# Performance work log

Measured on AMD Instinct MI355X. Metric: run time of the kernel, lower is better.

Reference implementation:

```python
import jax, jax.numpy as jnp
import numpy as np

N = 50000          # number of nodes / output rows (len(degs))
IN_C, OUT_C = 16, 16
EDGE_F = 13        # edge feature dim fed to filter net
HID = 32           # filter-net hidden width
E_NOMINAL = 800000 # target number of edges (sum of degs)


def setup_inputs() -> dict:
    rng = np.random.default_rng(0)
    # variable per-node degrees in [0, 32], adjusted so they sum exactly to E_NOMINAL
    degs = rng.integers(0, 33, size=N).astype(np.int64)
    degs[0] = max(0, degs[0] + (E_NOMINAL - int(degs.sum())))
    E = int(degs.sum())
    # segment id of each edge = destination node (equivalent to the degs-driven loop)
    idxd = np.repeat(np.arange(N, dtype=np.int32), degs)
    idxn = rng.integers(0, N, size=E).astype(np.int32)  # source node gather index

    key = jax.random.key(0)
    k1, k2, k3, k4 = jax.random.split(key, 4)
    x = jax.random.normal(k1, (N, IN_C), jnp.float32)
    edgefeats = jax.random.normal(k2, (E, EDGE_F), jnp.float32)
    # filter net: Linear(EDGE_F->HID) -> ReLU -> Linear(HID->IN_C*OUT_C)
    W1 = jax.random.normal(k3, (EDGE_F, HID), jnp.float32) / np.float32(np.sqrt(EDGE_F))
    b1 = jnp.zeros((HID,), jnp.float32)
    W2 = jax.random.normal(k4, (HID, IN_C * OUT_C), jnp.float32) / np.float32(np.sqrt(HID))
    b2 = jnp.zeros((IN_C * OUT_C,), jnp.float32)
    return {
        "x": x, "edgefeats": edgefeats,
        "W1": W1, "b1": b1, "W2": W2, "b2": b2,
        "idxn": jnp.asarray(idxn), "idxd": jnp.asarray(idxd),
        "degs": jnp.asarray(degs.astype(np.float32)),
    }


def reference(x, edgefeats, W1, b1, W2, b2, idxn, idxd, degs):
    # filter net generates a per-edge [IN_C, OUT_C] weight matrix
    h = jax.nn.relu(edgefeats @ W1 + b1)                 # [E, HID]
    w = (h @ W2 + b2).reshape(-1, IN_C, OUT_C)           # [E, IN_C, OUT_C]
    # gather source-node features and apply per-edge matvec (bmm with [E,1,IN_C])
    sel = x[idxn]                                        # [E, IN_C]
    prod = jnp.einsum('ei,eio->eo', sel, w)              # [E, OUT_C]
    # segment-mean over each node's incoming edges; degree-0 nodes -> 0
    s = jax.ops.segment_sum(prod, idxd, num_segments=N)  # [N, OUT_C]
    d = degs[:, None]
    return jnp.where(d > 0, s / jnp.maximum(d, 1.0), jnp.float32(0.0))
```

## Files before the change

kernel.cpp:

```cpp
#include <hip/hip_runtime.h>

typedef _Float16 half2v __attribute__((ext_vector_type(2)));
typedef _Float16 half4v __attribute__((ext_vector_type(4)));
typedef _Float16 half8v __attribute__((ext_vector_type(8)));
typedef float   float4v __attribute__((ext_vector_type(4)));

#define INC     16
#define OUTC    16
#define EFN     13
#define HIDC    32
#define EPW     128
#define WPB     4
#define MAXSPAN 40

#define GLOBAL_AS __attribute__((address_space(1)))
#define LDS_AS    __attribute__((address_space(3)))

union H8 { half8v v; half2v h2[4]; };

__global__ __launch_bounds__(256) void prep(
    const float* __restrict__ W2,
    const float* __restrict__ x,
    _Float16*    __restrict__ wsB,
    _Float16*    __restrict__ wsXh,
    float*       __restrict__ out,
    int nh)
{
    const int b = blockIdx.x;
    if (b < 32) {
        const int i = b * 256 + threadIdx.x;
        const int j = i & 7;
        const int l = (i >> 3) & 63;
        const int t = i >> 9;
        const int q = l >> 4, n = l & 15;
        const int kk = (j < 4) ? (q * 4 + j) : (16 + q * 4 + (j & 3));
        wsB[i] = (_Float16)W2[kk * 256 + t * 16 + n];
    } else {
        const int i = (b - 32) * 256 + threadIdx.x;
        if (i * 4 < nh)
            ((float4*)out)[i] = make_float4(0, 0, 0, 0);
        if (i * 8 < nh) {
            const float4 v0 = ((const float4*)x)[i * 2];
            const float4 v1 = ((const float4*)x)[i * 2 + 1];
            half8v h;
            h[0] = (_Float16)v0.x; h[1] = (_Float16)v0.y;
            h[2] = (_Float16)v0.z; h[3] = (_Float16)v0.w;
            h[4] = (_Float16)v1.x; h[5] = (_Float16)v1.y;
            h[6] = (_Float16)v1.z; h[7] = (_Float16)v1.w;
            *(half8v*)(wsXh + (size_t)i * 8) = h;
        }
    }
}

__global__ __launch_bounds__(256, 3) void edge_kernel(
    const _Float16* __restrict__ xh,
    const float* __restrict__ edgefeats,
    const float* __restrict__ W1,
    const float* __restrict__ b1,
    const float* __restrict__ b2,
    const int*   __restrict__ idxn,
    const int*   __restrict__ idxd,
    const float* __restrict__ degs,
    const _Float16* __restrict__ wsB,
    float*       __restrict__ out,
    int E)
{
    __shared__ __align__(16) float sEF[WPB][EPW * EFN];
    __shared__ __align__(16) int   sidxn[WPB][EPW];
    __shared__ float lacc[WPB][MAXSPAN * OUTC];

    const int tid  = threadIdx.x;
    const int lane = tid & 63;
    const int wid  = tid >> 6;
    const int n    = lane & 15;
    const int q    = lane >> 4;

    const long vw = (long)blockIdx.x * WPB + wid;
    const long b0 = vw * EPW;
    if (b0 >= (long)E) return;
    const long bEnd = (b0 + EPW < (long)E) ? (b0 + EPW) : (long)E;
    const bool full = (b0 + EPW <= (long)E);
    const long Em1  = (long)E - 1;

    float* sEF_w   = sEF[wid];
    int*   sidxn_w = sidxn[wid];
    float* lacc_w  = lacc[wid];

    const long ea = b0 + n, eb = b0 + 16 + n;
    const int nd0 = idxn[(ea <= Em1) ? ea : Em1];
    const int nd1 = idxn[(eb <= Em1) ? eb : Em1];
    __builtin_amdgcn_sched_barrier(0);

    if (full) {
        const char* efsrc = (const char*)edgefeats + (size_t)b0 * (EFN * 4);
        #pragma unroll
        for (int c = 0; c < 6; ++c)
            __builtin_amdgcn_global_load_lds(
                (const GLOBAL_AS unsigned int*)(efsrc + c * 1024 + lane * 16),
                (LDS_AS unsigned int*)((char*)sEF_w + c * 1024), 16, 0, 0);
        if (lane < 32) {
            __builtin_amdgcn_global_load_lds(
                (const GLOBAL_AS unsigned int*)(efsrc + 6144 + lane * 16),
                (LDS_AS unsigned int*)((char*)sEF_w + 6144), 16, 0, 0);
            __builtin_amdgcn_global_load_lds(
                (const GLOBAL_AS unsigned int*)((const char*)(idxn + b0) + lane * 16),
                (LDS_AS unsigned int*)sidxn_w, 16, 0, 0);
        }
    } else {
        const long mx = (long)E * EFN - 1;
        for (int i = lane; i < EPW * EFN; i += 64) {
            long gi = b0 * EFN + i;
            if (gi > mx) gi = mx;
            sEF_w[i] = edgefeats[gi];
        }
        for (int i = lane; i < EPW; i += 64) {
            long e = b0 + i;
            if (e > Em1) e = Em1;
            sidxn_w[i] = idxn[e];
        }
    }
    __builtin_amdgcn_sched_barrier(0);

    const int d_lo = idxd[b0];
    const int d_hi = idxd[bEnd - 1];
    const int span = d_hi - d_lo;

    H8 bfr[16];
    #pragma unroll
    for (int t = 0; t < 16; ++t)
        bfr[t].v = *(const half8v*)(wsB + ((size_t)(t * 64 + lane) * 8));

    #pragma unroll
    for (int it = 0; it < MAXSPAN * OUTC / 64; ++it) lacc_w[lane + it * 64] = 0.0f;

    half4v a1, a2;
    float4v c1, c2;
    #pragma unroll
    for (int jj = 0; jj < 4; ++jj) {
        const int f = q * 4 + jj;
        const bool ok = (f < EFN);
        a1[jj] = ok ? (_Float16)W1[f * HIDC + n]      : (_Float16)0.f;
        a2[jj] = ok ? (_Float16)W1[f * HIDC + 16 + n] : (_Float16)0.f;
        c1[jj] = b1[q * 4 + jj];
        c2[jj] = b1[16 + q * 4 + jj];
    }
    half8v bfragB2;
    #pragma unroll
    for (int j = 0; j < 8; ++j) {
        _Float16 val = (_Float16)0.f;
        if (q < 2) val = (_Float16)b2[(q * 8 + j) * 16 + n];
        bfragB2[j] = val;
    }

    const int f0i = (q < 3) ? (q * 4) : 9;

    half8v pxa0 = *(const half8v*)(xh + (size_t)nd0 * INC);
    half8v pxb0 = *(const half8v*)(xh + (size_t)nd0 * INC + 8);
    half8v pxa1 = *(const half8v*)(xh + (size_t)nd1 * INC);
    half8v pxb1 = *(const half8v*)(xh + (size_t)nd1 * INC + 8);
    __builtin_amdgcn_sched_barrier(0);

    asm volatile("s_waitcnt vmcnt(0) lgkmcnt(0)" ::: "memory");
    __builtin_amdgcn_sched_barrier(0);

    #pragma unroll
    for (int t16 = 0; t16 < 8; ++t16) {
        const long base = b0 + (long)t16 * 16;
        const bool vM   = (base + n < (long)E);

        const half8v xA = (t16 & 1) ? pxa1 : pxa0;
        const half8v xB = (t16 & 1) ? pxb1 : pxb0;
        if (t16 < 6) {
            const int ndn = sidxn_w[(t16 + 2) * 16 + n];
            if (t16 & 1) {
                pxa1 = *(const half8v*)(xh + (size_t)ndn * INC);
                pxb1 = *(const half8v*)(xh + (size_t)ndn * INC + 8);
            } else {
                pxa0 = *(const half8v*)(xh + (size_t)ndn * INC);
                pxb0 = *(const half8v*)(xh + (size_t)ndn * INC + 8);
            }
        }
        long de = base + q * 4;
        if (de > (long)E - 4) de = (long)E - 4;
        const int4 dd = *(const int4*)(idxd + de);
        __builtin_amdgcn_sched_barrier(0);

        const float* efp = sEF_w + (size_t)(t16 * 16 + n) * EFN + f0i;
        const float e0 = efp[0], e1 = efp[1], e2 = efp[2], e3 = efp[3];

        H8 sa, sb_;
        sa.v = xA; sb_.v = xB;
        const half2v zz = {(_Float16)0.f, (_Float16)0.f};
        half2v selh[8];
        #pragma unroll
        for (int i = 0; i < 4; ++i) {
            selh[i]     = vM ? sa.h2[i]  : zz;
            selh[4 + i] = vM ? sb_.h2[i] : zz;
        }

        half4v efB;
        if (q < 3) {
            efB[0] = (_Float16)e0; efB[1] = (_Float16)e1;
            efB[2] = (_Float16)e2; efB[3] = (_Float16)e3;
        } else {
            efB[0] = (_Float16)e3; efB[1] = (_Float16)0.f;
            efB[2] = (_Float16)0.f; efB[3] = (_Float16)0.f;
        }

        const float4v hf1 = __builtin_amdgcn_mfma_f32_16x16x16f16(a1, efB, c1, 0, 0, 0);
        const float4v hf2 = __builtin_amdgcn_mfma_f32_16x16x16f16(a2, efB, c2, 0, 0, 0);

        H8 hu;
        #pragma unroll
        for (int r = 0; r < 2; ++r) {
            half2v t1 = {(_Float16)fmaxf(hf1[2*r], 0.f), (_Float16)fmaxf(hf1[2*r+1], 0.f)};
            half2v t2 = {(_Float16)fmaxf(hf2[2*r], 0.f), (_Float16)fmaxf(hf2[2*r+1], 0.f)};
            hu.h2[r]     = t1;
            hu.h2[2 + r] = t2;
        }

        float4v acc = {0.f, 0.f, 0.f, 0.f};
        #pragma unroll
        for (int t = 0; t < 16; ++t) {
            _Float16 sv = (t & 1) ? selh[t >> 1][1] : selh[t >> 1][0];
            half2v sb = {sv, sv};
            H8 a;
            a.h2[0] = sb * hu.h2[0];
            a.h2[1] = sb * hu.h2[1];
            a.h2[2] = sb * hu.h2[2];
            a.h2[3] = sb * hu.h2[3];
            acc = __builtin_amdgcn_mfma_f32_16x16x32_f16(a.v, bfr[t].v, acc, 0, 0, 0);
        }
        {
            H8 a;
            #pragma unroll
            for (int j2 = 0; j2 < 4; ++j2) {
                a.h2[j2] = (q < 2) ? selh[q * 4 + j2] : zz;
            }
            acc = __builtin_amdgcn_mfma_f32_16x16x32_f16(a.v, bfragB2, acc, 0, 0, 0);
        }

        const int r0 = ((dd.x < d_hi) ? dd.x : d_hi) - d_lo;
        const int r1 = ((dd.y < d_hi) ? dd.y : d_hi) - d_lo;
        const int r2 = ((dd.z < d_hi) ? dd.z : d_hi) - d_lo;
        const int r3 = ((dd.w < d_hi) ? dd.w : d_hi) - d_lo;
        if (r0 == r3) {
            atomicAdd(&lacc_w[r0 * OUTC + n], acc[0] + acc[1] + acc[2] + acc[3]);
        } else {
            atomicAdd(&lacc_w[r0 * OUTC + n], acc[0]);
            atomicAdd(&lacc_w[r1 * OUTC + n], acc[1]);
            atomicAdd(&lacc_w[r2 * OUTC + n], acc[2]);
            atomicAdd(&lacc_w[r3 * OUTC + n], acc[3]);
        }
    }

    asm volatile("s_waitcnt lgkmcnt(0)" ::: "memory");

    const bool first_starts = (b0 == 0)        || (idxd[b0 - 1] != d_lo);
    const bool last_ends    = (bEnd == (long)E) || (idxd[bEnd]   != d_hi);

    for (int i = lane; i < (span + 1) * OUTC; i += 64) {
        const int u = i >> 4;
        const int o = i & 15;
        const int v = d_lo + u;
        const float bin = lacc_w[u * OUTC + o];
        const bool starts = (u > 0)    || first_starts;
        const bool ends   = (u < span) || last_ends;
        const float dg = degs[v];
        const float val = (dg > 0.0f) ? bin / dg : 0.0f;
        if (starts && ends) {
            out[(size_t)v * OUTC + o] = val;
        } else {
            atomicAdd(&out[(size_t)v * OUTC + o], val);
        }
    }
}

extern "C" void kernel_launch(void* const* d_in, const int* in_sizes, int n_in,
                              void* d_out, int out_size, void* d_ws, size_t ws_size,
                              hipStream_t stream)
{
    const float* x         = (const float*)d_in[0];
    const float* edgefeats = (const float*)d_in[1];
    const float* W1        = (const float*)d_in[2];
    const float* b1        = (const float*)d_in[3];
    const float* W2        = (const float*)d_in[4];
    const float* b2        = (const float*)d_in[5];
    const int*   idxn      = (const int*)d_in[6];
    const int*   idxd      = (const int*)d_in[7];
    const float* degs      = (const float*)d_in[8];

    const int E = in_sizes[6];
    const int N = in_sizes[8];
    const int nvw   = (E + EPW - 1) / EPW;
    const int gridw = (nvw + WPB - 1) / WPB;
    const int nh = N * INC;

    _Float16* wsB  = (_Float16*)d_ws;
    _Float16* wsXh = (_Float16*)((char*)d_ws + 16384);

    const int zblocks = (nh / 4 + 255) / 256;
    prep<<<32 + zblocks, 256, 0, stream>>>(W2, x, wsB, wsXh, (float*)d_out, nh);

    edge_kernel<<<gridw, 256, 0, stream>>>(wsXh, edgefeats, W1, b1, b2,
                                           idxn, idxd, degs, wsB,
                                           (float*)d_out, E);
}
```

Measured before the change: 158.1 us.

## Double edges per wave to 256 and loop tiles with paired prefetch macro

Each wave now processes 256 edges instead of 128 (16 tiles of 16). The edge-feature async copy grows to 13 full chunks, and the per-tile body becomes a macro invoked in a non-unrolled loop over tile pairs with double-buffered x prefetch. Launch bounds drop from 3 to 2 blocks per CU to fit the larger LDS footprint, and MAXSPAN rises to 48. The aim is to amortize per-wave setup (W1/W2 fragment loads, flush of local bins) over more edges, at the cost of occupancy and a higher risk of a wave's segment span overflowing the LDS bins.

Result: slower. 170.1 us (+7.6%).

```diff
diff --git a/kernel.cpp b/kernel.cpp
--- a/kernel.cpp
+++ b/kernel.cpp
@@ -9,9 +9,10 @@
 #define OUTC    16
 #define EFN     13
 #define HIDC    32
-#define EPW     128
+#define EPW     256
+#define NT      (EPW / 16)
 #define WPB     4
-#define MAXSPAN 40
+#define MAXSPAN 48
 
 #define GLOBAL_AS __attribute__((address_space(1)))
 #define LDS_AS    __attribute__((address_space(3)))
@@ -52,7 +53,86 @@
     }
 }
 
-__global__ __launch_bounds__(256, 3) void edge_kernel(
+#define DO_TILE(T16, PXA, PXB)                                               \
+  {                                                                          \
+    const long base = b0 + (long)(T16) * 16;                                 \
+    const bool vM   = (base + n < (long)E);                                  \
+    const half8v xA = PXA;                                                   \
+    const half8v xB = PXB;                                                   \
+    const int pft = (T16) + 2;                                               \
+    if (pft < NT) {                                                          \
+        const int ndn = sidxn_w[pft * 16 + n];                               \
+        PXA = *(const half8v*)(xh + (size_t)ndn * INC);                      \
+        PXB = *(const half8v*)(xh + (size_t)ndn * INC + 8);                  \
+    }                                                                        \
+    long de = base + q * 4;                                                  \
+    if (de > (long)E - 4) de = (long)E - 4;                                  \
+    const int4 dd = *(const int4*)(idxd + de);                               \
+    __builtin_amdgcn_sched_barrier(0);                                       \
+    const float* efp = sEF_w + (size_t)((T16) * 16 + n) * EFN + f0i;         \
+    const float e0 = efp[0], e1 = efp[1], e2 = efp[2], e3 = efp[3];          \
+    H8 sa, sb_;                                                              \
+    sa.v = xA; sb_.v = xB;                                                   \
+    const half2v zz = {(_Float16)0.f, (_Float16)0.f};                        \
+    half2v selh[8];                                                          \
+    _Pragma("unroll")                                                        \
+    for (int i = 0; i < 4; ++i) {                                            \
+        selh[i]     = vM ? sa.h2[i]  : zz;                                   \
+        selh[4 + i] = vM ? sb_.h2[i] : zz;                                   \
+    }                                                                        \
+    half4v efB;                                                              \
+    if (q < 3) {                                                             \
+        efB[0] = (_Float16)e0; efB[1] = (_Float16)e1;                        \
+        efB[2] = (_Float16)e2; efB[3] = (_Float16)e3;                        \
+    } else {                                                                 \
+        efB[0] = (_Float16)e3; efB[1] = (_Float16)0.f;                       \
+        efB[2] = (_Float16)0.f; efB[3] = (_Float16)0.f;                      \
+    }                                                                        \
+    const float4v hf1 = __builtin_amdgcn_mfma_f32_16x16x16f16(a1, efB, c1, 0, 0, 0); \
+    const float4v hf2 = __builtin_amdgcn_mfma_f32_16x16x16f16(a2, efB, c2, 0, 0, 0); \
+    H8 hu;                                                                   \
+    _Pragma("unroll")                                                        \
+    for (int r = 0; r < 2; ++r) {                                            \
+        half2v t1 = {(_Float16)fmaxf(hf1[2*r], 0.f), (_Float16)fmaxf(hf1[2*r+1], 0.f)}; \
+        half2v t2 = {(_Float16)fmaxf(hf2[2*r], 0.f), (_Float16)fmaxf(hf2[2*r+1], 0.f)}; \
+        hu.h2[r]     = t1;                                                   \
+        hu.h2[2 + r] = t2;                                                   \
+    }                                                                        \
+    float4v acc = {0.f, 0.f, 0.f, 0.f};                                      \
+    _Pragma("unroll")                                                        \
+    for (int t = 0; t < 16; ++t) {                                           \
+        _Float16 sv = (t & 1) ? selh[t >> 1][1] : selh[t >> 1][0];           \
+        half2v sb = {sv, sv};                                                \
+        H8 a;                                                                \
+        a.h2[0] = sb * hu.h2[0];                                             \
+        a.h2[1] = sb * hu.h2[1];                                             \
+        a.h2[2] = sb * hu.h2[2];                                             \
+        a.h2[3] = sb * hu.h2[3];                                             \
+        acc = __builtin_amdgcn_mfma_f32_16x16x32_f16(a.v, bfr[t].v, acc, 0, 0, 0); \
+    }                                                                        \
+    {                                                                        \
+        H8 a;                                                                \
+        _Pragma("unroll")                                                    \
+        for (int j2 = 0; j2 < 4; ++j2) {                                     \
+            a.h2[j2] = (q < 2) ? selh[q * 4 + j2] : zz;                      \
+        }                                                                    \
+        acc = __builtin_amdgcn_mfma_f32_16x16x32_f16(a.v, bfragB2, acc, 0, 0, 0); \
+    }                                                                        \
+    const int r0 = ((dd.x < d_hi) ? dd.x : d_hi) - d_lo;                     \
+    const int r1 = ((dd.y < d_hi) ? dd.y : d_hi) - d_lo;                     \
+    const int r2 = ((dd.z < d_hi) ? dd.z : d_hi) - d_lo;                     \
+    const int r3 = ((dd.w < d_hi) ? dd.w : d_hi) - d_lo;                     \
+    if (r0 == r3) {                                                          \
+        atomicAdd(&lacc_w[r0 * OUTC + n], acc[0] + acc[1] + acc[2] + acc[3]);\
+    } else {                                                                 \
+        atomicAdd(&lacc_w[r0 * OUTC + n], acc[0]);                           \
+        atomicAdd(&lacc_w[r1 * OUTC + n], acc[1]);                           \
+        atomicAdd(&lacc_w[r2 * OUTC + n], acc[2]);                           \
+        atomicAdd(&lacc_w[r3 * OUTC + n], acc[3]);                           \
+    }                                                                        \
+  }
+
+__global__ __launch_bounds__(256, 2) void edge_kernel(
     const _Float16* __restrict__ xh,
     const float* __restrict__ edgefeats,
     const float* __restrict__ W1,
@@ -94,18 +174,13 @@
     if (full) {
         const char* efsrc = (const char*)edgefeats + (size_t)b0 * (EFN * 4);
         #pragma unroll
-        for (int c = 0; c < 6; ++c)
+        for (int c = 0; c < 13; ++c)
             __builtin_amdgcn_global_load_lds(
                 (const GLOBAL_AS unsigned int*)(efsrc + c * 1024 + lane * 16),
                 (LDS_AS unsigned int*)((char*)sEF_w + c * 1024), 16, 0, 0);
-        if (lane < 32) {
-            __builtin_amdgcn_global_load_lds(
-                (const GLOBAL_AS unsigned int*)(efsrc + 6144 + lane * 16),
-                (LDS_AS unsigned int*)((char*)sEF_w + 6144), 16, 0, 0);
-            __builtin_amdgcn_global_load_lds(
-                (const GLOBAL_AS unsigned int*)((const char*)(idxn + b0) + lane * 16),
-                (LDS_AS unsigned int*)sidxn_w, 16, 0, 0);
-        }
+        __builtin_amdgcn_global_load_lds(
+            (const GLOBAL_AS unsigned int*)((const char*)(idxn + b0) + lane * 16),
+            (LDS_AS unsigned int*)sidxn_w, 16, 0, 0);
     } else {
         const long mx = (long)E * EFN - 1;
         for (int i = lane; i < EPW * EFN; i += 64) {
@@ -163,95 +238,9 @@
     asm volatile("s_waitcnt vmcnt(0) lgkmcnt(0)" ::: "memory");
     __builtin_amdgcn_sched_barrier(0);
 
-    #pragma unroll
-    for (int t16 = 0; t16 < 8; ++t16) {
-        const long base = b0 + (long)t16 * 16;
-        const bool vM   = (base + n < (long)E);
-
-        const half8v xA = (t16 & 1) ? pxa1 : pxa0;
-        const half8v xB = (t16 & 1) ? pxb1 : pxb0;
-        if (t16 < 6) {
-            const int ndn = sidxn_w[(t16 + 2) * 16 + n];
-            if (t16 & 1) {
-                pxa1 = *(const half8v*)(xh + (size_t)ndn * INC);
-                pxb1 = *(const half8v*)(xh + (size_t)ndn * INC + 8);
-            } else {
-                pxa0 = *(const half8v*)(xh + (size_t)ndn * INC);
-                pxb0 = *(const half8v*)(xh + (size_t)ndn * INC + 8);
-            }
-        }
-        long de = base + q * 4;
-        if (de > (long)E - 4) de = (long)E - 4;
-        const int4 dd = *(const int4*)(idxd + de);
-        __builtin_amdgcn_sched_barrier(0);
-
-        const float* efp = sEF_w + (size_t)(t16 * 16 + n) * EFN + f0i;
-        const float e0 = efp[0], e1 = efp[1], e2 = efp[2], e3 = efp[3];
-
-        H8 sa, sb_;
-        sa.v = xA; sb_.v = xB;
-        const half2v zz = {(_Float16)0.f, (_Float16)0.f};
-        half2v selh[8];
-        #pragma unroll
-        for (int i = 0; i < 4; ++i) {
-            selh[i]     = vM ? sa.h2[i]  : zz;
-            selh[4 + i] = vM ? sb_.h2[i] : zz;
-        }
-
-        half4v efB;
-        if (q < 3) {
-            efB[0] = (_Float16)e0; efB[1] = (_Float16)e1;
-            efB[2] = (_Float16)e2; efB[3] = (_Float16)e3;
-        } else {
-            efB[0] = (_Float16)e3; efB[1] = (_Float16)0.f;
-            efB[2] = (_Float16)0.f; efB[3] = (_Float16)0.f;
-        }
-
-        const float4v hf1 = __builtin_amdgcn_mfma_f32_16x16x16f16(a1, efB, c1, 0, 0, 0);
-        const float4v hf2 = __builtin_amdgcn_mfma_f32_16x16x16f16(a2, efB, c2, 0, 0, 0);
-
-        H8 hu;
-        #pragma unroll
-        for (int r = 0; r < 2; ++r) {
-            half2v t1 = {(_Float16)fmaxf(hf1[2*r], 0.f), (_Float16)fmaxf(hf1[2*r+1], 0.f)};
-            half2v t2 = {(_Float16)fmaxf(hf2[2*r], 0.f), (_Float16)fmaxf(hf2[2*r+1], 0.f)};
-            hu.h2[r]     = t1;
-            hu.h2[2 + r] = t2;
-        }
-
-        float4v acc = {0.f, 0.f, 0.f, 0.f};
-        #pragma unroll
-        for (int t = 0; t < 16; ++t) {
-            _Float16 sv = (t & 1) ? selh[t >> 1][1] : selh[t >> 1][0];
-            half2v sb = {sv, sv};
-            H8 a;
-            a.h2[0] = sb * hu.h2[0];
-            a.h2[1] = sb * hu.h2[1];
-            a.h2[2] = sb * hu.h2[2];
-            a.h2[3] = sb * hu.h2[3];
-            acc = __builtin_amdgcn_mfma_f32_16x16x32_f16(a.v, bfr[t].v, acc, 0, 0, 0);
-        }
-        {
-            H8 a;
-            #pragma unroll
-            for (int j2 = 0; j2 < 4; ++j2) {
-                a.h2[j2] = (q < 2) ? selh[q * 4 + j2] : zz;
-            }
-            acc = __builtin_amdgcn_mfma_f32_16x16x32_f16(a.v, bfragB2, acc, 0, 0, 0);
-        }
-
-        const int r0 = ((dd.x < d_hi) ? dd.x : d_hi) - d_lo;
-        const int r1 = ((dd.y < d_hi) ? dd.y : d_hi) - d_lo;
-        const int r2 = ((dd.z < d_hi) ? dd.z : d_hi) - d_lo;
-        const int r3 = ((dd.w < d_hi) ? dd.w : d_hi) - d_lo;
-        if (r0 == r3) {
-            atomicAdd(&lacc_w[r0 * OUTC + n], acc[0] + acc[1] + acc[2] + acc[3]);
-        } else {
-            atomicAdd(&lacc_w[r0 * OUTC + n], acc[0]);
-            atomicAdd(&lacc_w[r1 * OUTC + n], acc[1]);
-            atomicAdd(&lacc_w[r2 * OUTC + n], acc[2]);
-            atomicAdd(&lacc_w[r3 * OUTC + n], acc[3]);
-        }
+    for (int tt = 0; tt < NT; tt += 2) {
+        DO_TILE(tt,     pxa0, pxb0)
+        DO_TILE(tt + 1, pxa1, pxb1)
     }
 
     asm volatile("s_waitcnt lgkmcnt(0)" ::: "memory");
```
